# Kernel tuning notes

Measured on AMD Instinct MI355X. Metric: run time of the kernel, lower is better.

The kernel has to match this reference:

```python
import jax, jax.numpy as jnp
import numpy as np

POOLING_COUNTS = [15, 8, 8]
N_CLIPS = 64


def build_mask_and_indices(pooling_counts, N):
    """Replicates the static index construction in __init__ (pure numpy)."""
    mask2d = np.zeros((N, N), dtype=bool)
    mask2d[np.arange(N), np.arange(N)] = True
    maskij = []
    pool_specs = []  # (kernel, stride) for each level
    for gi, c in enumerate(pooling_counts):
        if gi == 0:
            pool_specs.extend([(2, 1)] * c)
        else:
            pool_specs.extend([(3, 2)] + [(2, 1)] * (c - 1))
    stride, offset = 1, 0
    for c in pooling_counts:
        for _ in range(c):
            offset += stride
            i = np.arange(0, N - offset, stride)
            j = np.arange(offset, N, stride)
            mask2d[i, j] = True
            maskij.append((i, j))
        stride *= 2
    return mask2d, maskij, pool_specs


def maxpool1d(x, k, s):
    # x: [B, D, L]; MaxPool1d(kernel=k, stride=s), no padding
    L = x.shape[-1]
    out_len = (L - k) // s + 1
    idx = np.arange(out_len)[:, None] * s + np.arange(k)[None, :]  # [out_len, k]
    return x[..., idx].max(axis=-1)


def setup_inputs() -> dict:
    key = jax.random.key(0)
    x = jax.random.normal(key, (16, 512, N_CLIPS), dtype=jnp.float32)
    return {"x": x}


def reference(x):
    B, D, N = x.shape
    mask2d_np, maskij, pool_specs = build_mask_and_indices(POOLING_COUNTS, N)
    diag = np.arange(N)

    # diagonal scatter: map2d[:, :, n, n] = x[:, :, n]
    base = jnp.zeros((B, D, N, N), dtype=x.dtype).at[:, :, diag, diag].set(x)

    # boundary map: average of endpoint features at each (i, j) line
    boundary_map2d = base
    for i, j in maskij:
        boundary_map2d = boundary_map2d.at[:, :, i, j].set((x[:, :, i] + x[:, :, j]) * 0.5)

    # content map: pyramid of max-pools scattered onto the same lines
    content_map2d = base
    xp = x
    for (k, s), (i, j) in zip(pool_specs, maskij):
        xp = maxpool1d(xp, k, s)
        content_map2d = content_map2d.at[:, :, i, j].set(xp)

    mask2d = jnp.broadcast_to(jnp.asarray(mask2d_np)[None, None], (B, 1, N, N))
    return boundary_map2d, content_map2d, mask2d
```

## Files before the change

### kernel.cpp

```cpp
#include <hip/hip_runtime.h>


__device__ __forceinline__ bool on_line(int i, int off) {
    return (off <= 15)
        || ((off & 1) && off >= 17 && off <= 31 && !(i & 1))
        || (((off & 3) == 3) && off >= 35 && !(i & 3));
}

__global__ __launch_bounds__(256) void sbc_kernel(const float* __restrict__ x,
                                                  float* __restrict__ out,
                                                  size_t mapsz) {
    __shared__ float sp[7][64];
    const int bd = blockIdx.x;
    const int t  = threadIdx.x;

    if (t < 64) sp[0][t] = x[(size_t)bd * 64 + t];
    __syncthreads();
#pragma unroll
    for (int k = 1; k < 7; ++k) {
        if (t < 64) {
            const int w = 1 << (k - 1);
            float v = sp[k - 1][t];
            if (t + w < 64) v = fmaxf(v, sp[k - 1][t + w]);
            sp[k][t] = v;
        }
        __syncthreads();
    }

    const size_t bbase = (size_t)bd * 4096;
#pragma unroll
    for (int it = 0; it < 4; ++it) {
        const int p4 = t + it * 256;
        const int p  = p4 << 2;
        const int i  = p >> 6;
        const int j0 = p & 63;
        const float xi = sp[0][i];
        float bb[4], cc[4];
#pragma unroll
        for (int q = 0; q < 4; ++q) {
            const int j = j0 + q;
            float b = 0.0f, c = 0.0f;
            if (j == i) {
                b = xi; c = xi;
            } else if (j > i) {
                const int off = j - i;
                if (on_line(i, off)) {
                    b = 0.5f * (xi + sp[0][j]);
                    const int k = 31 - __clz(off + 1);
                    c = fmaxf(sp[k][i], sp[k][j + 1 - (1 << k)]);
                }
            }
            bb[q] = b; cc[q] = c;
        }
        *(float4*)(out + bbase + p)         = make_float4(bb[0], bb[1], bb[2], bb[3]);
        *(float4*)(out + mapsz + bbase + p) = make_float4(cc[0], cc[1], cc[2], cc[3]);
    }

    if ((bd & 511) == 0) {
        const int b = bd >> 9;
        float* mout = out + 2 * mapsz + (size_t)b * 4096;
#pragma unroll
        for (int it = 0; it < 4; ++it) {
            const int p4 = t + it * 256;
            const int p  = p4 << 2;
            const int i  = p >> 6;
            const int j0 = p & 63;
            float mm[4];
#pragma unroll
            for (int q = 0; q < 4; ++q) {
                const int j = j0 + q;
                bool on = (j == i) || (j > i && on_line(i, j - i));
                mm[q] = on ? 1.0f : 0.0f;
            }
            *(float4*)(mout + p) = make_float4(mm[0], mm[1], mm[2], mm[3]);
        }
    }
}

extern "C" void kernel_launch(void* const* d_in, const int* in_sizes, int n_in,
                              void* d_out, int out_size, void* d_ws, size_t ws_size,
                              hipStream_t stream) {
    const float* x = (const float*)d_in[0];
    float* out = (float*)d_out;
    const int N  = 64;
    const int BD = in_sizes[0] / N;
    const size_t mapsz = (size_t)BD * N * N;
    sbc_kernel<<<dim3(BD), dim3(256), 0, stream>>>(x, out, mapsz);
}
```

Before: 259.2 us.

## Batch eight rows per block with precomputed line offsets and shuffle pyramid

```diff
diff --git a/kernel.cpp b/kernel.cpp
--- a/kernel.cpp
+++ b/kernel.cpp
@@ -1,5 +1,8 @@
 #include <hip/hip_runtime.h>
 
+
+#define TPB 256
+#define T_TILES 8
 
 __device__ __forceinline__ bool on_line(int i, int off) {
     return (off <= 15)
@@ -7,72 +10,96 @@
         || (((off & 3) == 3) && off >= 35 && !(i & 3));
 }
 
-__global__ __launch_bounds__(256) void sbc_kernel(const float* __restrict__ x,
+__global__ __launch_bounds__(TPB) void sbc_kernel(const float* __restrict__ x,
                                                   float* __restrict__ out,
                                                   size_t mapsz) {
     __shared__ float sp[7][64];
-    const int bd = blockIdx.x;
-    const int t  = threadIdx.x;
+    const int t   = threadIdx.x;
+    const int bd0 = blockIdx.x * T_TILES;
 
-    if (t < 64) sp[0][t] = x[(size_t)bd * 64 + t];
-    __syncthreads();
+    int   ioff[4], joff[4];
+    int   c0off[4][4], c1off[4][4];
+    float s[4][4];
 #pragma unroll
-    for (int k = 1; k < 7; ++k) {
+    for (int g = 0; g < 4; ++g) {
+        const int p  = (t + g * 256) << 2;
+        const int i  = p >> 6;
+        const int j0 = p & 63;
+        ioff[g] = i << 2;
+        joff[g] = j0 << 2;
+#pragma unroll
+        for (int q = 0; q < 4; ++q) {
+            const int j = j0 + q;
+            const bool m = (j == i) || (j > i && on_line(i, j - i));
+            if (m) {
+                const int len = j - i + 1;
+                const int k   = 31 - __clz(len);
+                c0off[g][q] = (k << 8) + (i << 2);
+                c1off[g][q] = (k << 8) + ((j + 1 - (1 << k)) << 2);
+                s[g][q] = 0.5f;
+            } else {
+                c0off[g][q] = 0; c1off[g][q] = 0; s[g][q] = 0.0f;
+            }
+        }
+    }
+
+    float xv[T_TILES];
+    if (t < 64) {
+#pragma unroll
+        for (int tt = 0; tt < T_TILES; ++tt)
+            xv[tt] = x[(size_t)(bd0 + tt) * 64 + t];
+    }
+
+    const char* spb = (const char*)&sp[0][0];
+
+#pragma unroll
+    for (int tt = 0; tt < T_TILES; ++tt) {
         if (t < 64) {
-            const int w = 1 << (k - 1);
-            float v = sp[k - 1][t];
-            if (t + w < 64) v = fmaxf(v, sp[k - 1][t + w]);
-            sp[k][t] = v;
+            float v = xv[tt];
+            sp[0][t] = v;
+            int w = 1;
+#pragma unroll
+            for (int k = 1; k < 7; ++k) {
+                const float v2 = __shfl_down(v, w, 64);
+                v = fmaxf(v, v2);
+                sp[k][t] = v;
+                w <<= 1;
+            }
+        }
+        __syncthreads();
+
+        const size_t base = (size_t)(bd0 + tt) * 4096;
+#pragma unroll
+        for (int g = 0; g < 4; ++g) {
+            const int p = (t + g * 256) << 2;
+            const float  xi  = *(const float*)(spb + ioff[g]);
+            const float4 xj4 = *(const float4*)(spb + joff[g]);
+            float4 bv, cv;
+            bv.x = s[g][0] * (xi + xj4.x);
+            bv.y = s[g][1] * (xi + xj4.y);
+            bv.z = s[g][2] * (xi + xj4.z);
+            bv.w = s[g][3] * (xi + xj4.w);
+            cv.x = (s[g][0] + s[g][0]) * fmaxf(*(const float*)(spb + c0off[g][0]),
+                                               *(const float*)(spb + c1off[g][0]));
+            cv.y = (s[g][1] + s[g][1]) * fmaxf(*(const float*)(spb + c0off[g][1]),
+                                               *(const float*)(spb + c1off[g][1]));
+            cv.z = (s[g][2] + s[g][2]) * fmaxf(*(const float*)(spb + c0off[g][2]),
+                                               *(const float*)(spb + c1off[g][2]));
+            cv.w = (s[g][3] + s[g][3]) * fmaxf(*(const float*)(spb + c0off[g][3]),
+                                               *(const float*)(spb + c1off[g][3]));
+            *(float4*)(out + base + p)         = bv;
+            *(float4*)(out + mapsz + base + p) = cv;
         }
         __syncthreads();
     }
 
-    const size_t bbase = (size_t)bd * 4096;
+    if ((bd0 & 511) == 0) {
+        float* mout = out + 2 * mapsz + (size_t)(bd0 >> 9) * 4096;
 #pragma unroll
-    for (int it = 0; it < 4; ++it) {
-        const int p4 = t + it * 256;
-        const int p  = p4 << 2;
-        const int i  = p >> 6;
-        const int j0 = p & 63;
-        const float xi = sp[0][i];
-        float bb[4], cc[4];
-#pragma unroll
-        for (int q = 0; q < 4; ++q) {
-            const int j = j0 + q;
-            float b = 0.0f, c = 0.0f;
-            if (j == i) {
-                b = xi; c = xi;
-            } else if (j > i) {
-                const int off = j - i;
-                if (on_line(i, off)) {
-                    b = 0.5f * (xi + sp[0][j]);
-                    const int k = 31 - __clz(off + 1);
-                    c = fmaxf(sp[k][i], sp[k][j + 1 - (1 << k)]);
-                }
-            }
-            bb[q] = b; cc[q] = c;
-        }
-        *(float4*)(out + bbase + p)         = make_float4(bb[0], bb[1], bb[2], bb[3]);
-        *(float4*)(out + mapsz + bbase + p) = make_float4(cc[0], cc[1], cc[2], cc[3]);
-    }
-
-    if ((bd & 511) == 0) {
-        const int b = bd >> 9;
-        float* mout = out + 2 * mapsz + (size_t)b * 4096;
-#pragma unroll
-        for (int it = 0; it < 4; ++it) {
-            const int p4 = t + it * 256;
-            const int p  = p4 << 2;
-            const int i  = p >> 6;
-            const int j0 = p & 63;
-            float mm[4];
-#pragma unroll
-            for (int q = 0; q < 4; ++q) {
-                const int j = j0 + q;
-                bool on = (j == i) || (j > i && on_line(i, j - i));
-                mm[q] = on ? 1.0f : 0.0f;
-            }
-            *(float4*)(mout + p) = make_float4(mm[0], mm[1], mm[2], mm[3]);
+        for (int g = 0; g < 4; ++g) {
+            const int p = (t + g * 256) << 2;
+            *(float4*)(mout + p) = make_float4(s[g][0] + s[g][0], s[g][1] + s[g][1],
+                                               s[g][2] + s[g][2], s[g][3] + s[g][3]);
         }
     }
 }
@@ -85,5 +112,5 @@
     const int N  = 64;
     const int BD = in_sizes[0] / N;
     const size_t mapsz = (size_t)BD * N * N;
-    sbc_kernel<<<dim3(BD), dim3(256), 0, stream>>>(x, out, mapsz);
+    sbc_kernel<<<dim3(BD / T_TILES), dim3(TPB), 0, stream>>>(x, out, mapsz);
 }
```

Measured after the change: 255.3 us. Within noise of the previous version (-1.5%).
